# Kernel tuning notes

Hardware: AMD Instinct MI355X
Metric: run time of the kernel (lower is better)

## Reference

```python
import jax, jax.numpy as jnp
import numpy as np

# Geometry from the hard-coded `options` tensor
VIEWS, DETS = 160, 640
H, W = 416, 416
D_IMG = 0.006641            # image pixel size
D_DET = 0.012858            # detector bin size
ANG0 = 0.0
D_ANG = 0.009817477 * 4     # = 2*pi/160 (full scan)
S2R = 5.95                  # source-to-rotation-center distance
D2R = 4.906                 # detector-to-rotation-center distance
VIRDET = D_DET * S2R / (S2R + D2R)   # detector rescaled to isocenter (virtual detector)
PI = float(np.pi)
COEF = PI / VIEWS
BATCH = 32


def setup_inputs() -> dict:
    key = jax.random.key(0)
    projection = jax.random.normal(key, (BATCH, 1, VIEWS, DETS), dtype=jnp.float32)

    # Ramp filter (Ram-Lak, spatial domain), length 2*dets-1, exactly as in torch __init__
    x = np.arange(2 * DETS - 1) - DETS + 1
    x_safe = np.where(x == 0, 1, x).astype(np.float64)
    filt = np.where(np.abs(x) % 2 == 1,
                    -1.0 / (PI * PI * x_safe * x_safe * VIRDET * VIRDET),
                    0.0)
    filt[x == 0] = 1.0 / (4.0 * VIRDET * VIRDET)
    filt = jnp.asarray(filt.reshape(1, 1, 1, -1), dtype=jnp.float32)

    # Cosine (fan-beam) pre-weighting, detector bin centers at (i - dets/2 + 0.5)*virdet
    u = (np.arange(DETS) - DETS / 2 + 0.5) * VIRDET
    wv = S2R / np.sqrt(S2R ** 2 + u ** 2) * VIRDET
    w = jnp.asarray(wv.reshape(1, 1, 1, -1), dtype=jnp.float32)

    return {"projection": projection, "w": w, "filt": filt}


def _backproject(p):
    """Pixel-driven equidistant fan-beam backprojection.
    p: filtered sinogram [B, 1, VIEWS, DETS] -> recon [B, 1, H, W].
    """
    betas = ANG0 + D_ANG * jnp.arange(VIEWS, dtype=jnp.float32)
    xs = (jnp.arange(W, dtype=jnp.float32) - (W - 1) / 2.0) * D_IMG   # [W]
    ys = ((H - 1) / 2.0 - jnp.arange(H, dtype=jnp.float32)) * D_IMG   # [H]
    Xg, Yg = jnp.meshgrid(xs, ys)   # both [H, W]

    pv = jnp.moveaxis(p, 2, 0)  # [VIEWS, B, 1, DETS]

    def step(acc, inp):
        beta, pb = inp                      # pb: [B, 1, DETS]
        cb, sb = jnp.cos(beta), jnp.sin(beta)
        d = Xg * cb + Yg * sb               # pixel component toward source
        r = -Xg * sb + Yg * cb              # perpendicular component
        U = S2R - d                         # source-to-pixel depth
        # detector coordinate at isocenter -> fractional bin index
        idx = (S2R * r / U) / VIRDET + (DETS - 1) / 2.0   # [H, W]
        valid = (idx >= 0.0) & (idx <= DETS - 1)
        i0 = jnp.clip(jnp.floor(idx), 0, DETS - 2).astype(jnp.int32)
        frac = jnp.clip(idx - i0.astype(jnp.float32), 0.0, 1.0)
        # irregular gather + linear interpolation: [B,1,H,W]
        v = pb[:, :, i0] * (1.0 - frac) + pb[:, :, i0 + 1] * frac
        wgt = jnp.where(valid, (S2R / U) ** 2, 0.0)       # distance weighting
        return acc + wgt * v, None

    init = jnp.zeros((p.shape[0], 1, H, W), dtype=p.dtype)
    acc, _ = jax.lax.scan(step, init, (betas, pv))
    return acc


def reference(projection, w, filt):
    # 1) cosine weighting (elementwise broadcast over detector axis)
    p = projection * w
    p = jax.lax.conv_general_dilated(
        p, filt, window_strides=(1, 1),
        padding=((0, 0), (DETS - 1, DETS - 1)),
        dimension_numbers=("NCHW", "OIHW", "NCHW"))
    # 3) geometric backprojection + angular step normalization
    return COEF * _backproject(p)
```

## Files before the change

kernel.cpp:

```cpp
#include <hip/hip_runtime.h>

#define VIEWS 160
#define DETS  640
#define H_IMG 416
#define W_IMG 416
#define BATCH 32

constexpr double D_IMG_D  = 0.006641;
constexpr double D_DET_D  = 0.012858;
constexpr double S2R_D    = 5.95;
constexpr double D2R_D    = 4.906;
constexpr double VIRDET_D = D_DET_D * S2R_D / (S2R_D + D2R_D);
constexpr double PI_D     = 3.14159265358979323846;

typedef __fp16 __attribute__((ext_vector_type(2))) h2f;

__global__ __launch_bounds__(256) void viewconst_kernel(float* __restrict__ vcs) {
    int v = threadIdx.x;
    if (v >= VIEWS) return;
    float dang = (float)(0.009817477 * 4.0);
    float beta = dang * (float)v;
    float cb = cosf(beta), sb = sinf(beta);
    float K  = (float)(S2R_D / VIRDET_D);
    float p1 = -K * sb, p2 = K * cb;
    float* o = vcs + 8 * v;
    o[0] = cb; o[1] = sb; o[2] = p1; o[3] = p2;
    o[4] = cb * (float)D_IMG_D;
    o[5] = p1 * (float)D_IMG_D;
    o[6] = 0.f; o[7] = 0.f;
}

#define FT 320
#define RPAD 24
#define RSTR 209
__global__ __launch_bounds__(FT) void filter_kernel(
    const float* __restrict__ proj, const float* __restrict__ w,
    const float* __restrict__ filt, unsigned int* __restrict__ pf) {
    __shared__ float4 s_in[4 * RSTR];
    __shared__ float  s_f[2 * DETS];

    int t = threadIdx.x;
    int g = blockIdx.x;
    int group4 = g / 160;
    int v = g - group4 * 160;
    int g8 = group4 >> 1;
    int pairbase = (group4 & 1) * 2;

    for (int e = t; e < 4 * RSTR; e += FT) {
        int ri = e / RSTR, c4 = e - ri * RSTR;
        float4 pv = make_float4(0.f, 0.f, 0.f, 0.f);
        if (c4 >= RPAD && c4 < RPAD + 160) {
            int b = group4 * 4 + ri;
            pv = ((const float4*)(proj + ((size_t)b * VIEWS + v) * DETS))[c4 - RPAD];
            float4 wv = ((const float4*)w)[c4 - RPAD];
            pv.x *= wv.x; pv.y *= wv.y; pv.z *= wv.z; pv.w *= wv.w;
        }
        s_in[e] = pv;
    }
    for (int e = t; e < 2 * DETS; e += FT) s_f[e] = (e < 2 * DETS - 1) ? filt[e] : 0.f;
    __syncthreads();

    int sub = (t >= 160) ? 1 : 0;
    int tj  = t - sub * 160;

    const float4* f4  = (const float4*)s_f;
    const float4* in4 = &s_in[sub * 2 * RSTR + tj];
    float4 o0 = {0,0,0,0}, o1 = {0,0,0,0};
    float4 fp = f4[135];
    #pragma unroll 2
    for (int u = 0; u < 50; ++u) {
        float4 fn = f4[136 + u];
        {
            float4 iv = in4[0 * RSTR + u];
            o0.x = fmaf(iv.x, fp.w, o0.x); o0.x = fmaf(iv.y, fn.x, o0.x);
            o0.x = fmaf(iv.z, fn.y, o0.x); o0.x = fmaf(iv.w, fn.z, o0.x);
            o0.y = fmaf(iv.x, fp.z, o0.y); o0.y = fmaf(iv.y, fp.w, o0.y);
            o0.y = fmaf(iv.z, fn.x, o0.y); o0.y = fmaf(iv.w, fn.y, o0.y);
            o0.z = fmaf(iv.x, fp.y, o0.z); o0.z = fmaf(iv.y, fp.z, o0.z);
            o0.z = fmaf(iv.z, fp.w, o0.z); o0.z = fmaf(iv.w, fn.x, o0.z);
            o0.w = fmaf(iv.x, fp.x, o0.w); o0.w = fmaf(iv.y, fp.y, o0.w);
            o0.w = fmaf(iv.z, fp.z, o0.w); o0.w = fmaf(iv.w, fp.w, o0.w);
        }
        {
            float4 iv = in4[1 * RSTR + u];
            o1.x = fmaf(iv.x, fp.w, o1.x); o1.x = fmaf(iv.y, fn.x, o1.x);
            o1.x = fmaf(iv.z, fn.y, o1.x); o1.x = fmaf(iv.w, fn.z, o1.x);
            o1.y = fmaf(iv.x, fp.z, o1.y); o1.y = fmaf(iv.y, fp.w, o1.y);
            o1.y = fmaf(iv.z, fn.x, o1.y); o1.y = fmaf(iv.w, fn.y, o1.y);
            o1.z = fmaf(iv.x, fp.y, o1.z); o1.z = fmaf(iv.y, fp.z, o1.z);
            o1.z = fmaf(iv.z, fp.w, o1.z); o1.z = fmaf(iv.w, fn.x, o1.z);
            o1.w = fmaf(iv.x, fp.x, o1.w); o1.w = fmaf(iv.y, fp.y, o1.w);
            o1.w = fmaf(iv.z, fp.z, o1.w); o1.w = fmaf(iv.w, fp.w, o1.w);
        }
        fp = fn;
    }

    float coef = (float)((PI_D / (double)VIEWS) * S2R_D * S2R_D);
    auto h0 = __builtin_amdgcn_cvt_pkrtz(o0.x * coef, o1.x * coef);
    auto h1 = __builtin_amdgcn_cvt_pkrtz(o0.y * coef, o1.y * coef);
    auto h2 = __builtin_amdgcn_cvt_pkrtz(o0.z * coef, o1.z * coef);
    auto h3 = __builtin_amdgcn_cvt_pkrtz(o0.w * coef, o1.w * coef);
    uint4 pk = make_uint4(__builtin_bit_cast(unsigned int, h0),
                          __builtin_bit_cast(unsigned int, h1),
                          __builtin_bit_cast(unsigned int, h2),
                          __builtin_bit_cast(unsigned int, h3));
    unsigned int* dst = pf + ((size_t)g8 * VIEWS + v) * 2560
                           + (size_t)(pairbase + sub) * 640 + 4 * tj;
    *(uint4*)dst = pk;
}

__device__ __forceinline__ void gld_lds16(const char* g, char* l) {
    __builtin_amdgcn_global_load_lds(
        (const __attribute__((address_space(1))) unsigned int*)g,
        (__attribute__((address_space(3))) unsigned int*)l, 16, 0, 0);
}

#define PART_FLOATS ((size_t)BATCH * H_IMG * W_IMG)

__global__ __launch_bounds__(256, 8) void bp_kernel(
    const unsigned int* __restrict__ pf, const float* __restrict__ vcs,
    float* __restrict__ part) {
    __shared__ alignas(16) char s_buf[2 * 10240];

    int t    = threadIdx.x;
    int g8   = blockIdx.z >> 1;
    int half = blockIdx.z & 1;
    int x0   = blockIdx.x * 32 + (t & 15) * 2;
    int y    = blockIdx.y * 16 + (t >> 4);

    float X0 = ((float)x0 - 207.5f) * (float)D_IMG_D;
    float Yv = (207.5f - (float)y) * (float)D_IMG_D;

    float acc[8][2];
    #pragma unroll
    for (int b = 0; b < 8; ++b) { acc[b][0] = 0.f; acc[b][1] = 0.f; }
    h2f hacc[4][2];
    #pragma unroll
    for (int p = 0; p < 4; ++p) { hacc[p][0] = (h2f)0.f; hacc[p][1] = (h2f)0.f; }

    const float4* vc4 = (const float4*)vcs;
    int vbase = half * 80;
    const char* pf_base = (const char*)pf + ((size_t)g8 * VIEWS + vbase) * 10240;
    char* lds = s_buf;
    int wvbase  = (t >> 6) << 10;
    int laneoff = t * 16;

    #define STAGE(c)  do { \
        const char* src = pf_base + (size_t)(c) * 10240; \
        char* dst = lds + ((c) & 1) * 10240; \
        gld_lds16(src + laneoff, dst + wvbase); \
        gld_lds16(src + 4096 + laneoff, dst + 4096 + wvbase); \
        if (t < 128) gld_lds16(src + 8192 + laneoff, dst + 8192 + wvbase); \
    } while (0)

    STAGE(0);
    __syncthreads();

    for (int c = 0; c < 80; ++c) {
        if (c + 1 < 80) STAGE(c + 1);

        const unsigned int* vb = (const unsigned int*)(lds + (c & 1) * 10240);
        int v = vbase + c;
        float4 a  = vc4[2 * v];
        float4 bb = vc4[2 * v + 1];
        float U   = fmaf(-X0, a.x, fmaf(-Yv, a.y, (float)S2R_D));
        float num = fmaf(X0, a.z, Yv * a.w);
        #pragma unroll
        for (int k = 0; k < 2; ++k) {
            float ru   = __builtin_amdgcn_rcpf(U);
            float idx  = fmaf(num, ru, 319.5f);
            float idxc = __builtin_amdgcn_fmed3f(idx, 0.f, 639.f);
            float i0f  = fminf(idxc, 638.0f);
            int   i0   = (int)i0f;
            float frac = idxc - truncf(i0f);
            float w2   = ru * ru;
            float wgt  = (idx == idxc) ? w2 : 0.f;
            float w1f  = wgt * frac;
            float w0f  = wgt - w1f;
            h2f w0h = __builtin_amdgcn_cvt_pkrtz(w0f, w0f);
            h2f w1h = __builtin_amdgcn_cvt_pkrtz(w1f, w1f);
            const unsigned int* p0 = vb + i0;
            #pragma unroll
            for (int p = 0; p < 4; ++p) {
                unsigned int da = p0[p * 640];
                unsigned int db = p0[p * 640 + 1];
                h2f A = __builtin_bit_cast(h2f, da);
                h2f B = __builtin_bit_cast(h2f, db);
                hacc[p][k] = __builtin_elementwise_fma(A, w0h, hacc[p][k]);
                hacc[p][k] = __builtin_elementwise_fma(B, w1h, hacc[p][k]);
            }
            U   -= bb.x;
            num += bb.y;
        }
        if ((c & 7) == 7) {
            #pragma unroll
            for (int p = 0; p < 4; ++p)
                #pragma unroll
                for (int k = 0; k < 2; ++k) {
                    acc[2 * p][k]     += (float)hacc[p][k].x;
                    acc[2 * p + 1][k] += (float)hacc[p][k].y;
                    hacc[p][k] = (h2f)0.f;
                }
        }
        __syncthreads();
    }

    float* base = part + (size_t)half * PART_FLOATS;
    #pragma unroll
    for (int b = 0; b < 8; ++b) {
        float* op = base + ((size_t)(g8 * 8 + b) * H_IMG + y) * W_IMG + x0;
        *(float2*)op = make_float2(acc[b][0], acc[b][1]);
    }
}

__global__ __launch_bounds__(256) void merge_kernel(
    const float4* __restrict__ part, float4* __restrict__ out) {
    size_t i = (size_t)blockIdx.x * 256 + threadIdx.x;
    float4 a = part[i];
    float4 b = part[i + PART_FLOATS / 4];
    out[i] = make_float4(a.x + b.x, a.y + b.y, a.z + b.z, a.w + b.w);
}

extern "C" void kernel_launch(void* const* d_in, const int* in_sizes, int n_in,
                              void* d_out, int out_size, void* d_ws, size_t ws_size,
                              hipStream_t stream) {
    const float* proj = (const float*)d_in[0];
    const float* w    = (const float*)d_in[1];
    const float* filt = (const float*)d_in[2];
    float* out = (float*)d_out;

    float*        vcs  = (float*)d_ws;
    unsigned int* pf   = (unsigned int*)((char*)d_ws + 8192);
    float*        part = (float*)((char*)d_ws + 8192 + 6553600);

    viewconst_kernel<<<1, 256, 0, stream>>>(vcs);
    filter_kernel<<<(BATCH / 4) * VIEWS, FT, 0, stream>>>(proj, w, filt, pf);
    bp_kernel<<<dim3(13, 26, 8), 256, 0, stream>>>(pf, vcs, part);
    merge_kernel<<<(int)(PART_FLOATS / 4 / 256), 256, 0, stream>>>((const float4*)part, (float4*)out);
}
```

Before: 219.6 us.

## Backproject all 32 batches per block using per-tile detector windows

The backprojection now handles all 32 batch images per thread. For each tile and view it stages only a 64-bin detector window into LDS, using per-tile window starts precomputed by a new prep kernel from the tile corners. The filter output is re-laid out so each view interleaves all batches and the window is one contiguous load. The two view halves are combined with atomic adds into a zeroed output, which removes the partial buffer and the merge kernel. In exchange each thread holds 32 fp32 accumulators plus 16 packed half accumulators, occupancy drops to 6 waves, a memset is added, and results depend on the window fully covering each tile's footprint.

```diff
diff --git a/kernel.cpp b/kernel.cpp
--- a/kernel.cpp
+++ b/kernel.cpp
@@ -15,19 +15,38 @@
 
 typedef __fp16 __attribute__((ext_vector_type(2))) h2f;
 
-__global__ __launch_bounds__(256) void viewconst_kernel(float* __restrict__ vcs) {
-    int v = threadIdx.x;
-    if (v >= VIEWS) return;
+#define TILES_X 13
+#define TILES_Y 52
+#define NTILES  (TILES_X * TILES_Y)
+#define NB      64
+
+__global__ __launch_bounds__(160) void prep_kernel(float* __restrict__ vcs,
+                                                   int* __restrict__ bs_tab) {
+    int v    = threadIdx.x;
+    int tile = blockIdx.x;
     float dang = (float)(0.009817477 * 4.0);
     float beta = dang * (float)v;
     float cb = cosf(beta), sb = sinf(beta);
     float K  = (float)(S2R_D / VIRDET_D);
-    float p1 = -K * sb, p2 = K * cb;
-    float* o = vcs + 8 * v;
-    o[0] = cb; o[1] = sb; o[2] = p1; o[3] = p2;
-    o[4] = cb * (float)D_IMG_D;
-    o[5] = p1 * (float)D_IMG_D;
-    o[6] = 0.f; o[7] = 0.f;
+    if (tile == 0) {
+        ((float4*)vcs)[v] = make_float4(cb, sb, -K * sb, K * cb);
+    }
+    int ty = tile / TILES_X, tx = tile - ty * TILES_X;
+    float XL = ((float)(tx * 32) - 207.5f) * (float)D_IMG_D;
+    float XR = ((float)(tx * 32 + 31) - 207.5f) * (float)D_IMG_D;
+    float YT = (207.5f - (float)(ty * 8)) * (float)D_IMG_D;
+    float YB = (207.5f - (float)(ty * 8 + 7)) * (float)D_IMG_D;
+    float m = 1e30f;
+#define CORNER(Xc, Yc) { \
+        float r_ = -(Xc) * sb + (Yc) * cb; \
+        float U_ = (float)S2R_D - (Xc) * cb - (Yc) * sb; \
+        float ix = fmaf(K, r_ / U_, 319.5f); \
+        m = fminf(m, ix); }
+    CORNER(XL, YT); CORNER(XR, YT); CORNER(XL, YB); CORNER(XR, YB);
+#undef CORNER
+    int bs = (int)floorf(m) - 2;
+    bs = max(0, min(DETS - NB, bs)) & ~1;
+    bs_tab[tile * VIEWS + v] = bs;
 }
 
 #define FT 320
@@ -38,13 +57,12 @@
     const float* __restrict__ filt, unsigned int* __restrict__ pf) {
     __shared__ float4 s_in[4 * RSTR];
     __shared__ float  s_f[2 * DETS];
+    __shared__ unsigned int s_out[2 * DETS];
 
     int t = threadIdx.x;
     int g = blockIdx.x;
     int group4 = g / 160;
     int v = g - group4 * 160;
-    int g8 = group4 >> 1;
-    int pairbase = (group4 & 1) * 2;
 
     for (int e = t; e < 4 * RSTR; e += FT) {
         int ri = e / RSTR, c4 = e - ri * RSTR;
@@ -104,9 +122,13 @@
                           __builtin_bit_cast(unsigned int, h1),
                           __builtin_bit_cast(unsigned int, h2),
                           __builtin_bit_cast(unsigned int, h3));
-    unsigned int* dst = pf + ((size_t)g8 * VIEWS + v) * 2560
-                           + (size_t)(pairbase + sub) * 640 + 4 * tj;
-    *(uint4*)dst = pk;
+    *(uint4*)&s_out[sub * DETS + 4 * tj] = pk;
+    __syncthreads();
+
+    unsigned int a0 = s_out[2 * t],        a1 = s_out[2 * t + 1];
+    unsigned int b0 = s_out[DETS + 2 * t], b1 = s_out[DETS + 2 * t + 1];
+    uint4 o = make_uint4(a0, b0, a1, b1);
+    ((uint4*)(pf + ((size_t)v * 8 + group4) * (2 * DETS)))[t] = o;
 }
 
 __device__ __forceinline__ void gld_lds16(const char* g, char* l) {
@@ -115,110 +137,96 @@
         (__attribute__((address_space(3))) unsigned int*)l, 16, 0, 0);
 }
 
-#define PART_FLOATS ((size_t)BATCH * H_IMG * W_IMG)
-
-__global__ __launch_bounds__(256, 8) void bp_kernel(
+__global__ __launch_bounds__(256, 6) void bp_kernel(
     const unsigned int* __restrict__ pf, const float* __restrict__ vcs,
-    float* __restrict__ part) {
-    __shared__ alignas(16) char s_buf[2 * 10240];
+    const int* __restrict__ bs_tab, float* __restrict__ out) {
+    __shared__ alignas(16) unsigned int s_buf[2 * 8 * NB * 2];
 
     int t    = threadIdx.x;
-    int g8   = blockIdx.z >> 1;
-    int half = blockIdx.z & 1;
-    int x0   = blockIdx.x * 32 + (t & 15) * 2;
-    int y    = blockIdx.y * 16 + (t >> 4);
-
-    float X0 = ((float)x0 - 207.5f) * (float)D_IMG_D;
+    int half = blockIdx.z;
+    int tile = blockIdx.y * TILES_X + blockIdx.x;
+    int x    = blockIdx.x * 32 + (t & 31);
+    int y    = blockIdx.y * 8 + (t >> 5);
+
+    float X  = ((float)x - 207.5f) * (float)D_IMG_D;
     float Yv = (207.5f - (float)y) * (float)D_IMG_D;
 
-    float acc[8][2];
+    int vbase = half * (VIEWS / 2);
+    const float4* vc4 = (const float4*)vcs + vbase;
+    const int*    bsp = bs_tab + tile * VIEWS + vbase;
+    const char*   pfb = (const char*)pf + (size_t)vbase * 40960;
+    int  goff = (t >> 5) * (DETS * 8) + (t & 31) * 16;
+    char* ldst = (char*)s_buf + ((t >> 6) << 10);
+
+    float acc[32];
     #pragma unroll
-    for (int b = 0; b < 8; ++b) { acc[b][0] = 0.f; acc[b][1] = 0.f; }
-    h2f hacc[4][2];
+    for (int b = 0; b < 32; ++b) acc[b] = 0.f;
+    h2f hacc[16];
     #pragma unroll
-    for (int p = 0; p < 4; ++p) { hacc[p][0] = (h2f)0.f; hacc[p][1] = (h2f)0.f; }
-
-    const float4* vc4 = (const float4*)vcs;
-    int vbase = half * 80;
-    const char* pf_base = (const char*)pf + ((size_t)g8 * VIEWS + vbase) * 10240;
-    char* lds = s_buf;
-    int wvbase  = (t >> 6) << 10;
-    int laneoff = t * 16;
-
-    #define STAGE(c)  do { \
-        const char* src = pf_base + (size_t)(c) * 10240; \
-        char* dst = lds + ((c) & 1) * 10240; \
-        gld_lds16(src + laneoff, dst + wvbase); \
-        gld_lds16(src + 4096 + laneoff, dst + 4096 + wvbase); \
-        if (t < 128) gld_lds16(src + 8192 + laneoff, dst + 8192 + wvbase); \
-    } while (0)
-
-    STAGE(0);
+    for (int p = 0; p < 16; ++p) hacc[p] = (h2f)0.f;
+
+    float4 a0 = vc4[0];
+    int    bs = bsp[0];
+    float  U   = fmaf(-X, a0.x, fmaf(-Yv, a0.y, (float)S2R_D));
+    float  num = fmaf(X, a0.z, Yv * a0.w);
+    gld_lds16(pfb + (size_t)bs * 8 + goff, ldst);
     __syncthreads();
 
-    for (int c = 0; c < 80; ++c) {
-        if (c + 1 < 80) STAGE(c + 1);
-
-        const unsigned int* vb = (const unsigned int*)(lds + (c & 1) * 10240);
-        int v = vbase + c;
-        float4 a  = vc4[2 * v];
-        float4 bb = vc4[2 * v + 1];
-        float U   = fmaf(-X0, a.x, fmaf(-Yv, a.y, (float)S2R_D));
-        float num = fmaf(X0, a.z, Yv * a.w);
+    for (int c = 0; c < VIEWS / 2; ++c) {
+        float Un = U, numn = num; int bsn = bs;
+        if (c + 1 < VIEWS / 2) {
+            float4 an = vc4[c + 1];
+            bsn  = bsp[c + 1];
+            Un   = fmaf(-X, an.x, fmaf(-Yv, an.y, (float)S2R_D));
+            numn = fmaf(X, an.z, Yv * an.w);
+            gld_lds16(pfb + (size_t)(c + 1) * 40960 + (size_t)bsn * 8 + goff,
+                      ldst + (((c + 1) & 1) << 12));
+        }
+        float ru   = __builtin_amdgcn_rcpf(U);
+        float idx  = fmaf(num, ru, 319.5f);
+        float idxc = __builtin_amdgcn_fmed3f(idx, 0.f, 639.f);
+        float i0f  = fminf(idxc, 638.0f);
+        int   i0   = (int)i0f;
+        float frac = idxc - truncf(i0f);
+        float w2   = ru * ru;
+        float wgt  = (idx == idxc) ? w2 : 0.f;
+        float w1f  = wgt * frac;
+        float w0f  = wgt - w1f;
+        h2f w0h = __builtin_amdgcn_cvt_pkrtz(w0f, w0f);
+        h2f w1h = __builtin_amdgcn_cvt_pkrtz(w1f, w1f);
+        int bl = min(max(i0 - bs, 0), NB - 2);
+        const uint2* L = (const uint2*)((const char*)s_buf + ((c & 1) << 12)) + bl;
         #pragma unroll
-        for (int k = 0; k < 2; ++k) {
-            float ru   = __builtin_amdgcn_rcpf(U);
-            float idx  = fmaf(num, ru, 319.5f);
-            float idxc = __builtin_amdgcn_fmed3f(idx, 0.f, 639.f);
-            float i0f  = fminf(idxc, 638.0f);
-            int   i0   = (int)i0f;
-            float frac = idxc - truncf(i0f);
-            float w2   = ru * ru;
-            float wgt  = (idx == idxc) ? w2 : 0.f;
-            float w1f  = wgt * frac;
-            float w0f  = wgt - w1f;
-            h2f w0h = __builtin_amdgcn_cvt_pkrtz(w0f, w0f);
-            h2f w1h = __builtin_amdgcn_cvt_pkrtz(w1f, w1f);
-            const unsigned int* p0 = vb + i0;
-            #pragma unroll
-            for (int p = 0; p < 4; ++p) {
-                unsigned int da = p0[p * 640];
-                unsigned int db = p0[p * 640 + 1];
-                h2f A = __builtin_bit_cast(h2f, da);
-                h2f B = __builtin_bit_cast(h2f, db);
-                hacc[p][k] = __builtin_elementwise_fma(A, w0h, hacc[p][k]);
-                hacc[p][k] = __builtin_elementwise_fma(B, w1h, hacc[p][k]);
-            }
-            U   -= bb.x;
-            num += bb.y;
+        for (int gg = 0; gg < 8; ++gg) {
+            uint2 A = L[gg * NB];
+            uint2 B = L[gg * NB + 1];
+            h2f pa = __builtin_bit_cast(h2f, A.x);
+            h2f pb = __builtin_bit_cast(h2f, B.x);
+            h2f pc = __builtin_bit_cast(h2f, A.y);
+            h2f pd = __builtin_bit_cast(h2f, B.y);
+            hacc[2 * gg]     = __builtin_elementwise_fma(pa, w0h, hacc[2 * gg]);
+            hacc[2 * gg]     = __builtin_elementwise_fma(pb, w1h, hacc[2 * gg]);
+            hacc[2 * gg + 1] = __builtin_elementwise_fma(pc, w0h, hacc[2 * gg + 1]);
+            hacc[2 * gg + 1] = __builtin_elementwise_fma(pd, w1h, hacc[2 * gg + 1]);
         }
         if ((c & 7) == 7) {
             #pragma unroll
-            for (int p = 0; p < 4; ++p)
-                #pragma unroll
-                for (int k = 0; k < 2; ++k) {
-                    acc[2 * p][k]     += (float)hacc[p][k].x;
-                    acc[2 * p + 1][k] += (float)hacc[p][k].y;
-                    hacc[p][k] = (h2f)0.f;
-                }
+            for (int gg = 0; gg < 8; ++gg) {
+                acc[4 * gg + 0] += (float)hacc[2 * gg].x;
+                acc[4 * gg + 1] += (float)hacc[2 * gg].y;
+                acc[4 * gg + 2] += (float)hacc[2 * gg + 1].x;
+                acc[4 * gg + 3] += (float)hacc[2 * gg + 1].y;
+                hacc[2 * gg] = (h2f)0.f; hacc[2 * gg + 1] = (h2f)0.f;
+            }
         }
         __syncthreads();
-    }
-
-    float* base = part + (size_t)half * PART_FLOATS;
+        U = Un; num = numn; bs = bsn;
+    }
+
+    float* ob = out + (size_t)y * W_IMG + x;
     #pragma unroll
-    for (int b = 0; b < 8; ++b) {
-        float* op = base + ((size_t)(g8 * 8 + b) * H_IMG + y) * W_IMG + x0;
-        *(float2*)op = make_float2(acc[b][0], acc[b][1]);
-    }
-}
-
-__global__ __launch_bounds__(256) void merge_kernel(
-    const float4* __restrict__ part, float4* __restrict__ out) {
-    size_t i = (size_t)blockIdx.x * 256 + threadIdx.x;
-    float4 a = part[i];
-    float4 b = part[i + PART_FLOATS / 4];
-    out[i] = make_float4(a.x + b.x, a.y + b.y, a.z + b.z, a.w + b.w);
+    for (int b = 0; b < 32; ++b)
+        unsafeAtomicAdd(ob + (size_t)b * (H_IMG * W_IMG), acc[b]);
 }
 
 extern "C" void kernel_launch(void* const* d_in, const int* in_sizes, int n_in,
@@ -229,12 +237,12 @@
     const float* filt = (const float*)d_in[2];
     float* out = (float*)d_out;
 
-    float*        vcs  = (float*)d_ws;
-    unsigned int* pf   = (unsigned int*)((char*)d_ws + 8192);
-    float*        part = (float*)((char*)d_ws + 8192 + 6553600);
-
-    viewconst_kernel<<<1, 256, 0, stream>>>(vcs);
+    float*        vcs    = (float*)d_ws;
+    int*          bs_tab = (int*)((char*)d_ws + 4096);
+    unsigned int* pf     = (unsigned int*)((char*)d_ws + 4096 + 432640);
+
+    hipMemsetAsync(d_out, 0, (size_t)BATCH * H_IMG * W_IMG * sizeof(float), stream);
+    prep_kernel<<<NTILES, 160, 0, stream>>>(vcs, bs_tab);
     filter_kernel<<<(BATCH / 4) * VIEWS, FT, 0, stream>>>(proj, w, filt, pf);
-    bp_kernel<<<dim3(13, 26, 8), 256, 0, stream>>>(pf, vcs, part);
-    merge_kernel<<<(int)(PART_FLOATS / 4 / 256), 256, 0, stream>>>((const float4*)part, (float4*)out);
-}
+    bp_kernel<<<dim3(TILES_X, TILES_Y, 2), 256, 0, stream>>>(pf, vcs, bs_tab, out);
+}
```

After: 196.9 us. -10.3%, faster.
